# Performance work log

Hardware: AMD Instinct MI355X
Metric: run time of the kernel (lower is better)

## Reference

```python
import jax, jax.numpy as jnp
import numpy as np


def _conv2d_same(x, w, b):
    # x: [B,H,W,Cin], w: [kh,kw,Cin,Cout] (Keras HWIO), b: [Cout]
    y = jax.lax.conv_general_dilated(
        x, w, window_strides=(1, 1), padding='SAME',
        dimension_numbers=('NHWC', 'HWIO', 'NHWC'))
    return y + b


def _bilateral_slice_apply(grid, guide, image):
    # HDRNet bilateral_slice_apply with has_offset=True.
    # grid:  [B, gh, gw, gd, (ci+1)*co]
    # guide: [B, H, W] in [0,1]
    # image: [B, H, W, ci]
    B, gh, gw, gd, nc = grid.shape
    _, H, W, ci = image.shape
    co = nc // (ci + 1)
    dt = grid.dtype

    # Continuous grid coordinates (HDRNet convention: pixel centers, -0.5 shift)
    gx = (jnp.arange(W, dtype=dt) + 0.5) * gw / W - 0.5          # [W]
    gy = (jnp.arange(H, dtype=dt) + 0.5) * gh / H - 0.5          # [H]
    gz = guide.astype(dt) * gd - 0.5                             # [B,H,W]

    fx = jnp.floor(gx)
    fy = jnp.floor(gy)
    fz = jnp.floor(gz)
    bidx = jnp.arange(B)[:, None, None]                          # [B,1,1]

    coeffs = jnp.zeros((B, H, W, nc), dtype=dt)
    for dz in (0, 1):
        zz = fz + dz
        wz = jnp.maximum(1.0 - jnp.abs(gz - zz), 0.0)            # [B,H,W]
        zi = jnp.clip(zz.astype(jnp.int32), 0, gd - 1)           # [B,H,W]
        for dy in (0, 1):
            yy = fy + dy
            wy = jnp.maximum(1.0 - jnp.abs(gy - yy), 0.0)        # [H]
            yi = jnp.clip(yy.astype(jnp.int32), 0, gh - 1)       # [H]
            for dx in (0, 1):
                xx = fx + dx
                wx = jnp.maximum(1.0 - jnp.abs(gx - xx), 0.0)    # [W]
                xi = jnp.clip(xx.astype(jnp.int32), 0, gw - 1)   # [W]
                corner = grid[bidx, yi[None, :, None], xi[None, None, :], zi]  # [B,H,W,nc]
                w = wz * wy[None, :, None] * wx[None, None, :]   # [B,H,W]
                coeffs = coeffs + corner * w[..., None]

    # Per-pixel affine transform: coeffs -> [B,H,W,co,ci+1]
    A = coeffs.reshape(B, H, W, co, ci + 1)
    return jnp.einsum('bhwoi,bhwi->bhwo', A[..., :ci], image) + A[..., ci]


def setup_inputs() -> dict:
    key = jax.random.key(0)
    k1, k2, k3, k4 = jax.random.split(key, 4)
    B, H, W = 4, 1024, 1024
    grid = jax.random.normal(k1, (B, 16, 16, 8, 12), dtype=jnp.float32)
    guide = jax.random.uniform(k2, (B, H, W), dtype=jnp.float32)
    image = jax.random.normal(k3, (B, H, W, 3), dtype=jnp.float32)
    conv_w = jax.random.normal(k4, (3, 3, 3, 3), dtype=jnp.float32) * 0.1
    conv_b = jnp.zeros((3,), dtype=jnp.float32)
    return {'grid': grid, 'guide': guide, 'image': image,
            'conv_w': conv_w, 'conv_b': conv_b}


def reference(grid, guide, image, conv_w, conv_b):
    x = _conv2d_same(image, conv_w, conv_b)
    return _bilateral_slice_apply(grid, guide, x)
```

## Files before the change

### kernel.cpp

```cpp
#include <hip/hip_runtime.h>

#define H_  1024
#define W_  1024
#define B_  4
#define GH  16
#define GW  16
#define GD  8
#define NC  12
#define CELLF (GD * NC)
#define YROWF (GW * CELLF)

#define TW 64
#define TH 8
#define ROWF 198
#define WVALID (4 * ROWF)
#define WFLOATS (13 * 64)

typedef _Float16 h2 __attribute__((ext_vector_type(2)));

__device__ __forceinline__ h2 u2h(unsigned int u) { return __builtin_bit_cast(h2, u); }

__device__ __forceinline__ void gload_lds4(const float* g, float* l) {
    auto gp = (const __attribute__((address_space(1))) float*)g;
    auto lp = (__attribute__((address_space(3))) float*)l;
    __builtin_amdgcn_global_load_lds(gp, lp, 4, 0, 0);
}

__device__ __forceinline__ void conv3r(const float* a, const float* b, const float* c,
                                       float* acc, const float* wgt,
                                       float bias0, float bias1, float bias2) {
    acc[0] = bias0; acc[1] = bias1; acc[2] = bias2;
    const float* rows[3] = {a, b, c};
    #pragma unroll
    for (int kh = 0; kh < 3; ++kh)
        #pragma unroll
        for (int kw = 0; kw < 3; ++kw)
            #pragma unroll
            for (int ci = 0; ci < 3; ++ci) {
                float v = rows[kh][kw * 3 + ci];
                const float* wb = wgt + ((kh * 3 + kw) * 3 + ci) * 3;
                acc[0] += v * wb[0];
                acc[1] += v * wb[1];
                acc[2] += v * wb[2];
            }
}

__global__ __launch_bounds__(256, 8)
void fused_conv_slice(const float* __restrict__ grid,
                      const float* __restrict__ guide,
                      const float* __restrict__ image,
                      const float* __restrict__ conv_w,
                      const float* __restrict__ conv_b,
                      float* __restrict__ out)
{
    __shared__ float s_img[4][WFLOATS];
    __shared__ uint4 s_t128[TH][3 * GD];
    __shared__ uint2 s_t64[TH][3 * GD];

    const int tx  = threadIdx.x;
    const int tyq = threadIdx.y;
    const int bx  = blockIdx.x;
    const int by  = blockIdx.y;
    const int b   = blockIdx.z;
    const int x0 = bx * TW;
    const int y0 = by * TH;
    const int tid = tyq * 64 + tx;
    const int lr = tyq * 2;
    const float* ib = image + b * (H_ * W_ * 3);

    int cells[3];
    cells[0] = max(bx - 1, 0);
    cells[1] = bx;
    cells[2] = min(bx + 1, GW - 1);
    const float* gB = grid + b * (GH * GW * GD * NC);
    {
        int rr = tid >> 5;
        int le = tid & 31;
        int y  = y0 + rr;
        float gyf = (y + 0.5f) * (1.0f / 64.0f) - 0.5f;
        float fyf = floorf(gyf);
        float tyw = gyf - fyf;
        int iy = (int)fyf;
        int yi0 = min(max(iy, 0), GH - 1);
        int yi1 = min(max(iy + 1, 0), GH - 1);
        float wy0 = 1.0f - tyw, wy1 = tyw;
        const float4* G0 = (const float4*)(gB + yi0 * YROWF);
        const float4* G1 = (const float4*)(gB + yi1 * YROWF);
        #pragma unroll
        for (int k = 0; k < 3; ++k) {
            int e = le + k * 32;
            if (e < 72) {
                int s  = (e >= 48) ? 2 : ((e >= 24) ? 1 : 0);
                int re = e - s * 24;
                int z  = re / 3;
                int c4 = re - z * 3;
                int off = cells[s] * 24 + re;
                float4 v0 = G0[off], v1 = G1[off];
                h2 p0, p1;
                p0.x = (_Float16)(wy0 * v0.x + wy1 * v1.x);
                p0.y = (_Float16)(wy0 * v0.y + wy1 * v1.y);
                p1.x = (_Float16)(wy0 * v0.z + wy1 * v1.z);
                p1.y = (_Float16)(wy0 * v0.w + wy1 * v1.w);
                uint2 u;
                u.x = __builtin_bit_cast(unsigned int, p0);
                u.y = __builtin_bit_cast(unsigned int, p1);
                int ci = s * GD + z;
                unsigned short* dst = (c4 == 2)
                    ? (unsigned short*)&s_t64[rr][ci]
                    : (unsigned short*)&s_t128[rr][ci] + c4 * 4;
                *(uint2*)dst = u;
            }
        }
    }

    const int wr0 = y0 + lr - 1;
    const bool edge = (bx == 0) | (bx == (W_ / TW - 1)) |
                      (by == 0) | (by == (H_ / TH - 1));
    if (!edge) {
        #pragma unroll
        for (int i = 0; i < 13; ++i) {
            int f  = i * 64 + tx;
            int fe = min(f, WVALID - 1);
            int r  = fe / ROWF;
            int off = fe - r * ROWF;
            const float* src = ib + ((wr0 + r) * W_ + (x0 - 1)) * 3 + off;
            gload_lds4(src, &s_img[tyq][i * 64]);
        }
    } else {
        #pragma unroll
        for (int i = 0; i < 5; ++i) {
            int p = i * 64 + tx;
            if (p < 264) {
                int r = p / 66;
                int c = p - r * 66;
                int yy = wr0 + r;
                int xx = x0 - 1 + c;
                float v[3] = {0.f, 0.f, 0.f};
                if (((unsigned)yy < (unsigned)H_) && ((unsigned)xx < (unsigned)W_))
                    __builtin_memcpy(v, ib + (yy * W_ + xx) * 3, 12);
                float* d = &s_img[tyq][r * ROWF + c * 3];
                d[0] = v[0]; d[1] = v[1]; d[2] = v[2];
            }
        }
    }

    const int x = x0 + tx;
    const int guidebase = b * (H_ * W_);
    float g2[2];
    #pragma unroll
    for (int j = 0; j < 2; ++j)
        g2[j] = guide[guidebase + (y0 + lr + j) * W_ + x];

    float wgt[81];
    #pragma unroll
    for (int i = 0; i < 81; ++i) wgt[i] = conv_w[i];
    float bias0 = conv_b[0], bias1 = conv_b[1], bias2 = conv_b[2];

    __asm__ __volatile__("s_waitcnt vmcnt(0) lgkmcnt(0)" ::: "memory");
    __builtin_amdgcn_sched_barrier(0);

    auto ldr9 = [&](int r, float* d) {
        __builtin_memcpy(d, &s_img[tyq][r * ROWF + tx * 3], 36);
    };
    float ra[9], rb[9], rc[9];
    float acc2r[2][3];
    ldr9(0, ra);
    ldr9(1, rb);
    ldr9(2, rc);
    conv3r(ra, rb, rc, acc2r[0], wgt, bias0, bias1, bias2);
    ldr9(3, ra);
    conv3r(rb, rc, ra, acc2r[1], wgt, bias0, bias1, bias2);

    float gxf = (x + 0.5f) * (1.0f / 64.0f) - 0.5f;
    float fxf = floorf(gxf);
    float txw = gxf - fxf;
    float wxa = 1.0f - txw, wxb = txw;
    int s0 = (int)fxf - (bx - 1);

    const int outbase = b * (H_ * W_ * 3);

    #pragma unroll
    for (int j = 0; j < 2; ++j) {
        int y = y0 + lr + j;
        const uint4* T128 = &s_t128[lr + j][0];
        const uint2* T64  = &s_t64[lr + j][0];

        float gzf = g2[j] * 8.0f - 0.5f;
        float fzf = floorf(gzf);
        float tz = gzf - fzf;
        int iz = (int)fzf;
        int zb = min(max(iz, 0), GD - 2);
        float wA = (iz < 0) ? 1.0f : ((iz > GD - 2) ? 0.0f : (1.0f - tz));
        float wB = 1.0f - wA;

        float m0 = wxa * wA, m1 = wxa * wB, m2 = wxb * wA, m3 = wxb * wB;
        h2 m0h = {(_Float16)m0, (_Float16)m0};
        h2 m1h = {(_Float16)m1, (_Float16)m1};
        h2 m2h = {(_Float16)m2, (_Float16)m2};
        h2 m3h = {(_Float16)m3, (_Float16)m3};

        int ci0 = s0 * GD + zb;
        uint4 Alo = T128[ci0];          uint2 Ahi = T64[ci0];
        uint4 Blo = T128[ci0 + 1];      uint2 Bhi = T64[ci0 + 1];
        uint4 Clo = T128[ci0 + GD];     uint2 Chi = T64[ci0 + GD];
        uint4 Dlo = T128[ci0 + GD + 1]; uint2 Dhi = T64[ci0 + GD + 1];

        h2 A[6]  = {u2h(Alo.x), u2h(Alo.y), u2h(Alo.z), u2h(Alo.w), u2h(Ahi.x), u2h(Ahi.y)};
        h2 Bv[6] = {u2h(Blo.x), u2h(Blo.y), u2h(Blo.z), u2h(Blo.w), u2h(Bhi.x), u2h(Bhi.y)};
        h2 Cv[6] = {u2h(Clo.x), u2h(Clo.y), u2h(Clo.z), u2h(Clo.w), u2h(Chi.x), u2h(Chi.y)};
        h2 Dv[6] = {u2h(Dlo.x), u2h(Dlo.y), u2h(Dlo.z), u2h(Dlo.w), u2h(Dhi.x), u2h(Dhi.y)};

        h2 c[6];
        #pragma unroll
        for (int k = 0; k < 6; ++k)
            c[k] = __builtin_elementwise_fma(A[k], m0h,
                   __builtin_elementwise_fma(Bv[k], m1h,
                   __builtin_elementwise_fma(Cv[k], m2h, Dv[k] * m3h)));

        float a0 = acc2r[j][0], a1 = acc2r[j][1], a2 = acc2r[j][2];
        h2 q01 = {(_Float16)a0, (_Float16)a1};
        h2 q21 = {(_Float16)a2, (_Float16)1.0f};

        int oidx = outbase + (y * W_ + x) * 3;
        #pragma unroll
        for (int o3 = 0; o3 < 3; ++o3) {
            float t = __builtin_amdgcn_fdot2(c[2 * o3 + 1], q21, 0.0f, false);
            out[oidx + o3] = __builtin_amdgcn_fdot2(c[2 * o3], q01, t, false);
        }
    }
}

extern "C" void kernel_launch(void* const* d_in, const int* in_sizes, int n_in,
                              void* d_out, int out_size, void* d_ws, size_t ws_size,
                              hipStream_t stream) {
    const float* grid   = (const float*)d_in[0];
    const float* guide  = (const float*)d_in[1];
    const float* image  = (const float*)d_in[2];
    const float* conv_w = (const float*)d_in[3];
    const float* conv_b = (const float*)d_in[4];
    float* out = (float*)d_out;

    dim3 block(64, 4, 1);
    dim3 grid_dim(W_ / TW, H_ / TH, B_);
    fused_conv_slice<<<grid_dim, block, 0, stream>>>(grid, guide, image, conv_w, conv_b, out);
}
```

Measured before the change: 137.2 us.

## Process four rows per wave to cut conv halo reloads and grid prep

Each wave now computes four output rows instead of two, so the block tile grows from 8 to 16 rows and the 3x3 conv halo overhead per output row falls from 2/2 to 2/4 rows. Grid y-interpolation is restructured so each thread handles a whole cell's 12 coefficients with three float4 loads per row, written per wave, with padded LDS row stride. Launch bounds drop to 5 waves' occupancy hint, trading occupancy and register pressure for fewer redundant image loads and fewer blocks.

```diff
diff --git a/kernel.cpp b/kernel.cpp
--- a/kernel.cpp
+++ b/kernel.cpp
@@ -11,10 +11,9 @@
 #define YROWF (GW * CELLF)
 
 #define TW 64
-#define TH 8
-#define ROWF 198
-#define WVALID (4 * ROWF)
-#define WFLOATS (13 * 64)
+#define WROWS 4
+#define TH 16
+#define RSTR 200
 
 typedef _Float16 h2 __attribute__((ext_vector_type(2)));
 
@@ -45,7 +44,7 @@
             }
 }
 
-__global__ __launch_bounds__(256, 8)
+__global__ __launch_bounds__(256, 5)
 void fused_conv_slice(const float* __restrict__ grid,
                       const float* __restrict__ guide,
                       const float* __restrict__ image,
@@ -53,9 +52,9 @@
                       const float* __restrict__ conv_b,
                       float* __restrict__ out)
 {
-    __shared__ float s_img[4][WFLOATS];
+    __shared__ float s_img[4][6][RSTR];
     __shared__ uint4 s_t128[TH][3 * GD];
-    __shared__ uint2 s_t64[TH][3 * GD];
+    __shared__ uint2 s_t64 [TH][3 * GD];
 
     const int tx  = threadIdx.x;
     const int tyq = threadIdx.y;
@@ -64,73 +63,27 @@
     const int b   = blockIdx.z;
     const int x0 = bx * TW;
     const int y0 = by * TH;
-    const int tid = tyq * 64 + tx;
-    const int lr = tyq * 2;
+    const int yw0 = y0 + tyq * WROWS;
+    const int wr0 = yw0 - 1;
     const float* ib = image + b * (H_ * W_ * 3);
-
-    int cells[3];
-    cells[0] = max(bx - 1, 0);
-    cells[1] = bx;
-    cells[2] = min(bx + 1, GW - 1);
     const float* gB = grid + b * (GH * GW * GD * NC);
-    {
-        int rr = tid >> 5;
-        int le = tid & 31;
-        int y  = y0 + rr;
-        float gyf = (y + 0.5f) * (1.0f / 64.0f) - 0.5f;
-        float fyf = floorf(gyf);
-        float tyw = gyf - fyf;
-        int iy = (int)fyf;
-        int yi0 = min(max(iy, 0), GH - 1);
-        int yi1 = min(max(iy + 1, 0), GH - 1);
-        float wy0 = 1.0f - tyw, wy1 = tyw;
-        const float4* G0 = (const float4*)(gB + yi0 * YROWF);
-        const float4* G1 = (const float4*)(gB + yi1 * YROWF);
-        #pragma unroll
-        for (int k = 0; k < 3; ++k) {
-            int e = le + k * 32;
-            if (e < 72) {
-                int s  = (e >= 48) ? 2 : ((e >= 24) ? 1 : 0);
-                int re = e - s * 24;
-                int z  = re / 3;
-                int c4 = re - z * 3;
-                int off = cells[s] * 24 + re;
-                float4 v0 = G0[off], v1 = G1[off];
-                h2 p0, p1;
-                p0.x = (_Float16)(wy0 * v0.x + wy1 * v1.x);
-                p0.y = (_Float16)(wy0 * v0.y + wy1 * v1.y);
-                p1.x = (_Float16)(wy0 * v0.z + wy1 * v1.z);
-                p1.y = (_Float16)(wy0 * v0.w + wy1 * v1.w);
-                uint2 u;
-                u.x = __builtin_bit_cast(unsigned int, p0);
-                u.y = __builtin_bit_cast(unsigned int, p1);
-                int ci = s * GD + z;
-                unsigned short* dst = (c4 == 2)
-                    ? (unsigned short*)&s_t64[rr][ci]
-                    : (unsigned short*)&s_t128[rr][ci] + c4 * 4;
-                *(uint2*)dst = u;
-            }
-        }
-    }
-
-    const int wr0 = y0 + lr - 1;
+
     const bool edge = (bx == 0) | (bx == (W_ / TW - 1)) |
-                      (by == 0) | (by == (H_ / TH - 1));
+                      ((by == 0) & (tyq == 0)) | ((by == (H_ / TH - 1)) & (tyq == 3));
     if (!edge) {
         #pragma unroll
-        for (int i = 0; i < 13; ++i) {
-            int f  = i * 64 + tx;
-            int fe = min(f, WVALID - 1);
-            int r  = fe / ROWF;
-            int off = fe - r * ROWF;
-            const float* src = ib + ((wr0 + r) * W_ + (x0 - 1)) * 3 + off;
-            gload_lds4(src, &s_img[tyq][i * 64]);
+        for (int r = 0; r < 6; ++r) {
+            const float* rowbase = ib + ((wr0 + r) * W_ + (x0 - 1)) * 3;
+            gload_lds4(rowbase +   0 + tx, &s_img[tyq][r][0]);
+            gload_lds4(rowbase +  64 + tx, &s_img[tyq][r][64]);
+            gload_lds4(rowbase + 128 + tx, &s_img[tyq][r][128]);
+            gload_lds4(rowbase + 134 + tx, &s_img[tyq][r][134]);
         }
     } else {
         #pragma unroll
-        for (int i = 0; i < 5; ++i) {
+        for (int i = 0; i < 7; ++i) {
             int p = i * 64 + tx;
-            if (p < 264) {
+            if (p < 396) {
                 int r = p / 66;
                 int c = p - r * 66;
                 int yy = wr0 + r;
@@ -138,18 +91,59 @@
                 float v[3] = {0.f, 0.f, 0.f};
                 if (((unsigned)yy < (unsigned)H_) && ((unsigned)xx < (unsigned)W_))
                     __builtin_memcpy(v, ib + (yy * W_ + xx) * 3, 12);
-                float* d = &s_img[tyq][r * ROWF + c * 3];
+                float* d = &s_img[tyq][r][c * 3];
                 d[0] = v[0]; d[1] = v[1]; d[2] = v[2];
             }
         }
     }
 
+    #pragma unroll
+    for (int k = 0; k < 2; ++k) {
+        int cid = k * 64 + tx;
+        if (cid < WROWS * 24) {
+            int rr  = cid / 24;
+            int rem = cid - rr * 24;
+            int s   = rem >> 3;
+            int z   = rem & 7;
+            float gyf = (yw0 + rr + 0.5f) * (1.0f / 64.0f) - 0.5f;
+            float fyf = floorf(gyf);
+            float tyw = gyf - fyf;
+            int iy  = (int)fyf;
+            int yi0 = min(max(iy, 0), GH - 1);
+            int yi1 = min(max(iy + 1, 0), GH - 1);
+            float wy0 = 1.0f - tyw, wy1 = tyw;
+            int cellx = min(max(bx - 1 + s, 0), GW - 1);
+            const float4* G0 = (const float4*)(gB + yi0 * YROWF + cellx * CELLF + z * NC);
+            const float4* G1 = (const float4*)(gB + yi1 * YROWF + cellx * CELLF + z * NC);
+            float4 a0 = G0[0], a1 = G0[1], a2 = G0[2];
+            float4 c0 = G1[0], c1 = G1[1], c2 = G1[2];
+            h2 p0, p1, p2, p3, p4, p5;
+            p0.x = (_Float16)(wy0 * a0.x + wy1 * c0.x); p0.y = (_Float16)(wy0 * a0.y + wy1 * c0.y);
+            p1.x = (_Float16)(wy0 * a0.z + wy1 * c0.z); p1.y = (_Float16)(wy0 * a0.w + wy1 * c0.w);
+            p2.x = (_Float16)(wy0 * a1.x + wy1 * c1.x); p2.y = (_Float16)(wy0 * a1.y + wy1 * c1.y);
+            p3.x = (_Float16)(wy0 * a1.z + wy1 * c1.z); p3.y = (_Float16)(wy0 * a1.w + wy1 * c1.w);
+            p4.x = (_Float16)(wy0 * a2.x + wy1 * c2.x); p4.y = (_Float16)(wy0 * a2.y + wy1 * c2.y);
+            p5.x = (_Float16)(wy0 * a2.z + wy1 * c2.z); p5.y = (_Float16)(wy0 * a2.w + wy1 * c2.w);
+            uint4 lo;
+            lo.x = __builtin_bit_cast(unsigned int, p0);
+            lo.y = __builtin_bit_cast(unsigned int, p1);
+            lo.z = __builtin_bit_cast(unsigned int, p2);
+            lo.w = __builtin_bit_cast(unsigned int, p3);
+            uint2 hi;
+            hi.x = __builtin_bit_cast(unsigned int, p4);
+            hi.y = __builtin_bit_cast(unsigned int, p5);
+            int ci = s * GD + z;
+            s_t128[tyq * WROWS + rr][ci] = lo;
+            s_t64 [tyq * WROWS + rr][ci] = hi;
+        }
+    }
+
     const int x = x0 + tx;
     const int guidebase = b * (H_ * W_);
-    float g2[2];
-    #pragma unroll
-    for (int j = 0; j < 2; ++j)
-        g2[j] = guide[guidebase + (y0 + lr + j) * W_ + x];
+    float g4[4];
+    #pragma unroll
+    for (int j = 0; j < 4; ++j)
+        g4[j] = guide[guidebase + (yw0 + j) * W_ + x];
 
     float wgt[81];
     #pragma unroll
@@ -160,16 +154,18 @@
     __builtin_amdgcn_sched_barrier(0);
 
     auto ldr9 = [&](int r, float* d) {
-        __builtin_memcpy(d, &s_img[tyq][r * ROWF + tx * 3], 36);
+        __builtin_memcpy(d, &s_img[tyq][r][tx * 3], 36);
     };
     float ra[9], rb[9], rc[9];
-    float acc2r[2][3];
-    ldr9(0, ra);
-    ldr9(1, rb);
-    ldr9(2, rc);
-    conv3r(ra, rb, rc, acc2r[0], wgt, bias0, bias1, bias2);
+    float acc4[4][3];
+    ldr9(0, ra); ldr9(1, rb); ldr9(2, rc);
+    conv3r(ra, rb, rc, acc4[0], wgt, bias0, bias1, bias2);
     ldr9(3, ra);
-    conv3r(rb, rc, ra, acc2r[1], wgt, bias0, bias1, bias2);
+    conv3r(rb, rc, ra, acc4[1], wgt, bias0, bias1, bias2);
+    ldr9(4, rb);
+    conv3r(rc, ra, rb, acc4[2], wgt, bias0, bias1, bias2);
+    ldr9(5, rc);
+    conv3r(ra, rb, rc, acc4[3], wgt, bias0, bias1, bias2);
 
     float gxf = (x + 0.5f) * (1.0f / 64.0f) - 0.5f;
     float fxf = floorf(gxf);
@@ -180,12 +176,12 @@
     const int outbase = b * (H_ * W_ * 3);
 
     #pragma unroll
-    for (int j = 0; j < 2; ++j) {
-        int y = y0 + lr + j;
-        const uint4* T128 = &s_t128[lr + j][0];
-        const uint2* T64  = &s_t64[lr + j][0];
-
-        float gzf = g2[j] * 8.0f - 0.5f;
+    for (int j = 0; j < 4; ++j) {
+        int y = yw0 + j;
+        const uint4* T128 = &s_t128[tyq * WROWS + j][0];
+        const uint2* T64  = &s_t64 [tyq * WROWS + j][0];
+
+        float gzf = g4[j] * 8.0f - 0.5f;
         float fzf = floorf(gzf);
         float tz = gzf - fzf;
         int iz = (int)fzf;
@@ -217,7 +213,7 @@
                    __builtin_elementwise_fma(Bv[k], m1h,
                    __builtin_elementwise_fma(Cv[k], m2h, Dv[k] * m3h)));
 
-        float a0 = acc2r[j][0], a1 = acc2r[j][1], a2 = acc2r[j][2];
+        float a0 = acc4[j][0], a1 = acc4[j][1], a2 = acc4[j][2];
         h2 q01 = {(_Float16)a0, (_Float16)a1};
         h2 q21 = {(_Float16)a2, (_Float16)1.0f};
 
```

Result: no change. 137.0 us (-0.1%).
